# Performance work log

Measured on AMD Instinct MI355X. Metric: run time of the kernel, lower is better.

## Reference

```python
import jax, jax.numpy as jnp
import numpy as np

B, H, S, Dh = 2, 16, 2048, 64


def setup_inputs() -> dict:
    key = jax.random.key(0)
    kq, kk, kv = jax.random.split(key, 3)
    query = jax.random.normal(kq, (B, H, S, Dh), dtype=jnp.float32)
    k = jax.random.normal(kk, (B, H, S, Dh), dtype=jnp.float32)
    value = jax.random.normal(kv, (B, H, S, Dh), dtype=jnp.float32)
    mask = jnp.zeros((1, 1, S, S), dtype=jnp.float32)
    return {"query": query, "key": k, "value": value, "mask": mask}


def reference(query, key, value, mask):
    # scores: [B,H,S,S]
    dk = jnp.asarray(key.shape[-1], dtype=query.dtype)
    logits = jnp.einsum("bhqd,bhkd->bhqk", query, key) / jnp.sqrt(dk)
    logits = logits + mask * (-1e9)
    attention_weights = jax.nn.softmax(logits, axis=-1)
    output = jnp.einsum("bhqk,bhkd->bhqd", attention_weights, value)
    return (output, attention_weights)
```

## Files before the change

kernel.cpp:

```cpp
#include <hip/hip_runtime.h>
#include <hip/hip_bf16.h>
#include <stdint.h>

typedef __bf16 bf16;
typedef __attribute__((ext_vector_type(8))) __bf16 bf16x8;
typedef __attribute__((ext_vector_type(4))) float f32x4;

constexpr int S   = 2048;
constexpr int DH  = 64;
constexpr int BQ  = 16;
constexpr int NW  = 4;
constexpr int KPW = S / NW;
constexpr int NC  = KPW / 32;


__global__ __launch_bounds__(256)
void attn_fused(const float* __restrict__ Q, const float* __restrict__ K,
                const float* __restrict__ V, const float* __restrict__ Msk,
                float* __restrict__ Out, float* __restrict__ W)
{
    __shared__ float rs[NW][BQ];
    __shared__ float inv[BQ];
    __shared__ float opart[NW][BQ][DH];

    const int tid  = threadIdx.x;
    const int lane = tid & 63;
    const int wave = tid >> 6;
    const int c    = lane & 15;
    const int g    = lane >> 4;

    const int swz = (blockIdx.x & 7) * 512 + (blockIdx.x >> 3);
    const int bh = swz >> 7;
    const int q0 = (swz & 127) * BQ;

    const float* Qb = Q + (size_t)bh * S * DH;
    const float* Kb = K + (size_t)bh * S * DH;
    const float* Vb = V + (size_t)bh * S * DH;

    bf16x8 qlo, qhi;
    {
        const float* qr = Qb + (size_t)(q0 + c) * DH + g * 8;
        f32x4 a0 = *(const f32x4*)(qr);
        f32x4 a1 = *(const f32x4*)(qr + 4);
        f32x4 b0 = *(const f32x4*)(qr + 32);
        f32x4 b1 = *(const f32x4*)(qr + 36);
        #pragma unroll
        for (int j = 0; j < 4; ++j) {
            qlo[j]     = (bf16)a0[j];  qlo[j + 4] = (bf16)a1[j];
            qhi[j]     = (bf16)b0[j];  qhi[j + 4] = (bf16)b1[j];
        }
    }

    const int kbase = wave * KPW;
    const int cperm = 8 * (c >> 2) + (c & 3);
    const float* mrow = Msk + (size_t)(q0 + c) * S;

    bf16x8 pa[NC];
    float s = 0.f;
    #pragma unroll
    for (int kc = 0; kc < NC; ++kc) {
        const int k0 = kbase + kc * 32;
        const float* kr0 = Kb + (size_t)(k0 + cperm) * DH + g * 8;
        const float* kr1 = kr0 + (size_t)4 * DH;
        f32x4 a0 = *(const f32x4*)(kr0);
        f32x4 a1 = *(const f32x4*)(kr0 + 4);
        f32x4 b0 = *(const f32x4*)(kr0 + 32);
        f32x4 b1 = *(const f32x4*)(kr0 + 36);
        f32x4 a2 = *(const f32x4*)(kr1);
        f32x4 a3 = *(const f32x4*)(kr1 + 4);
        f32x4 b2 = *(const f32x4*)(kr1 + 32);
        f32x4 b3 = *(const f32x4*)(kr1 + 36);
        f32x4 m0 = *(const f32x4*)(mrow + k0 + 8 * g);
        f32x4 m1 = *(const f32x4*)(mrow + k0 + 8 * g + 4);

        bf16x8 kl0, kh0, kl1, kh1;
        #pragma unroll
        for (int j = 0; j < 4; ++j) {
            kl0[j] = (bf16)a0[j];  kl0[j + 4] = (bf16)a1[j];
            kh0[j] = (bf16)b0[j];  kh0[j + 4] = (bf16)b1[j];
            kl1[j] = (bf16)a2[j];  kl1[j + 4] = (bf16)a3[j];
            kh1[j] = (bf16)b2[j];  kh1[j + 4] = (bf16)b3[j];
        }
        f32x4 acc0 = {0.f, 0.f, 0.f, 0.f};
        f32x4 acc1 = {0.f, 0.f, 0.f, 0.f};
        acc0 = __builtin_amdgcn_mfma_f32_16x16x32_bf16(kl0, qlo, acc0, 0, 0, 0);
        acc0 = __builtin_amdgcn_mfma_f32_16x16x32_bf16(kh0, qhi, acc0, 0, 0, 0);
        acc1 = __builtin_amdgcn_mfma_f32_16x16x32_bf16(kl1, qlo, acc1, 0, 0, 0);
        acc1 = __builtin_amdgcn_mfma_f32_16x16x32_bf16(kh1, qhi, acc1, 0, 0, 0);

        #pragma unroll
        for (int r = 0; r < 4; ++r) {
            const float p0 = __expf(acc0[r] * 0.125f + m0[r] * (-1e9f));
            const float p1 = __expf(acc1[r] * 0.125f + m1[r] * (-1e9f));
            s += p0 + p1;
            pa[kc][r]     = (bf16)p0;
            pa[kc][r + 4] = (bf16)p1;
        }
    }

    s += __shfl_xor(s, 16);
    s += __shfl_xor(s, 32);
    if (lane < 16) rs[wave][lane] = s;
    __syncthreads();
    if (tid < BQ) {
        float t = 0.f;
        #pragma unroll
        for (int w = 0; w < NW; ++w) t += rs[w][tid];
        inv[tid] = 1.f / t;
    }
    __syncthreads();
    const float myinv = inv[c];

    f32x4 oacc[4] = {{0,0,0,0},{0,0,0,0},{0,0,0,0},{0,0,0,0}};
    float* Wrow = W + (size_t)bh * S * S + (size_t)(q0 + c) * S;

    #pragma unroll
    for (int kc = 0; kc < NC; ++kc) {
        const int k0 = kbase + kc * 32;

        const float* vp = Vb + (size_t)(k0 + 8 * g) * DH + c;
        float vv[4][8];
        #pragma unroll
        for (int j = 0; j < 8; ++j) {
            #pragma unroll
            for (int dt = 0; dt < 4; ++dt)
                vv[dt][j] = vp[j * DH + dt * 16];
        }

        f32x4 w0, w1;
        #pragma unroll
        for (int r = 0; r < 4; ++r) {
            w0[r] = (float)pa[kc][r]     * myinv;
            w1[r] = (float)pa[kc][r + 4] * myinv;
        }
        *(f32x4*)(Wrow + k0 + 8 * g)     = w0;
        *(f32x4*)(Wrow + k0 + 8 * g + 4) = w1;

        #pragma unroll
        for (int dt = 0; dt < 4; ++dt) {
            bf16x8 vb;
            #pragma unroll
            for (int j = 0; j < 8; ++j) vb[j] = (bf16)vv[dt][j];
            oacc[dt] = __builtin_amdgcn_mfma_f32_16x16x32_bf16(pa[kc], vb, oacc[dt], 0, 0, 0);
        }
    }

    #pragma unroll
    for (int dt = 0; dt < 4; ++dt)
        #pragma unroll
        for (int r = 0; r < 4; ++r)
            opart[wave][4 * g + r][16 * dt + c] = oacc[dt][r];
    __syncthreads();

    {
        const int q = tid >> 4;
        const int d = (tid & 15) * 4;
        f32x4 o = {0.f, 0.f, 0.f, 0.f};
        #pragma unroll
        for (int w = 0; w < NW; ++w) o += *(const f32x4*)&opart[w][q][d];
        const float is = inv[q];
        o.x *= is; o.y *= is; o.z *= is; o.w *= is;
        float* Ob = Out + ((size_t)bh * S + q0 + q) * DH + d;
        *(f32x4*)Ob = o;
    }
}

extern "C" void kernel_launch(void* const* d_in, const int* in_sizes, int n_in,
                              void* d_out, int out_size, void* d_ws, size_t ws_size,
                              hipStream_t stream) {
    const float* Q   = (const float*)d_in[0];
    const float* K   = (const float*)d_in[1];
    const float* V   = (const float*)d_in[2];
    const float* Msk = (const float*)d_in[3];

    float* Out = (float*)d_out;
    float* W   = Out + (size_t)2 * 16 * 2048 * 64;

    dim3 grid(32 * (S / BQ));
    dim3 block(256);
    hipLaunchKernelGGL(attn_fused, grid, block, 0, stream, Q, K, V, Msk, Out, W);
}
```

Baseline: 440.2 us.

## Pre-cast Q/K to bf16 and pre-transpose V in workspace before attention

Adds two preprocessing kernels: one converts K and Q to bf16, the other converts V to bf16 and transposes it to [bh][d][s]. The main attention kernel then loads bf16 operands directly with vector loads, including contiguous V^T rows for the PV MFMA. This removes the repeated fp32 loads and conversions of K and V, which every query block performs again, and the strided scalar V gathers. The cost is two extra kernel launches and an extra global round trip through workspace, and the old fp32 path is kept as a fallback when the workspace is too small.

Result: faster. 366.2 us (median of 2 runs) (-16.8%).

```diff
diff --git a/kernel.cpp b/kernel.cpp
--- a/kernel.cpp
+++ b/kernel.cpp
@@ -12,12 +12,199 @@
 constexpr int NW  = 4;
 constexpr int KPW = S / NW;
 constexpr int NC  = KPW / 32;
+constexpr int BH  = 32;
+constexpr size_t ELEMS = (size_t)BH * S * DH;
+constexpr size_t WS_NEED = ELEMS * 2 * 3;
 
 
 __global__ __launch_bounds__(256)
-void attn_fused(const float* __restrict__ Q, const float* __restrict__ K,
-                const float* __restrict__ V, const float* __restrict__ Msk,
-                float* __restrict__ Out, float* __restrict__ W)
+void cast_kq(const float* __restrict__ K, const float* __restrict__ Q,
+             bf16* __restrict__ Kb, bf16* __restrict__ Qb)
+{
+    const size_t t = (size_t)blockIdx.x * 256 + threadIdx.x;
+    {
+        const float* src = K + t * 8;
+        f32x4 a = *(const f32x4*)(src);
+        f32x4 b = *(const f32x4*)(src + 4);
+        bf16x8 o;
+        #pragma unroll
+        for (int j = 0; j < 4; ++j) { o[j] = (bf16)a[j]; o[j + 4] = (bf16)b[j]; }
+        *(bf16x8*)(Kb + t * 8) = o;
+    }
+    {
+        const float* src = Q + t * 8;
+        f32x4 a = *(const f32x4*)(src);
+        f32x4 b = *(const f32x4*)(src + 4);
+        bf16x8 o;
+        #pragma unroll
+        for (int j = 0; j < 4; ++j) { o[j] = (bf16)a[j]; o[j + 4] = (bf16)b[j]; }
+        *(bf16x8*)(Qb + t * 8) = o;
+    }
+}
+
+__global__ __launch_bounds__(256)
+void transpose_v(const float* __restrict__ V, bf16* __restrict__ Vt)
+{
+    __shared__ bf16 t[64][72];
+    const int bh = blockIdx.x >> 5;
+    const int sb = (blockIdx.x & 31) * 64;
+    const int tid = threadIdx.x;
+
+    {
+        const int r  = tid >> 2;
+        const int c0 = (tid & 3) * 16;
+        const float* src = V + ((size_t)bh * S + sb + r) * DH + c0;
+        f32x4 v0 = *(const f32x4*)(src);
+        f32x4 v1 = *(const f32x4*)(src + 4);
+        f32x4 v2 = *(const f32x4*)(src + 8);
+        f32x4 v3 = *(const f32x4*)(src + 12);
+        #pragma unroll
+        for (int j = 0; j < 4; ++j) {
+            t[r][c0 + j]      = (bf16)v0[j];
+            t[r][c0 + 4 + j]  = (bf16)v1[j];
+            t[r][c0 + 8 + j]  = (bf16)v2[j];
+            t[r][c0 + 12 + j] = (bf16)v3[j];
+        }
+    }
+    __syncthreads();
+    {
+        const int d  = tid >> 2;
+        const int s0 = (tid & 3) * 16;
+        bf16x8 o0, o1;
+        #pragma unroll
+        for (int j = 0; j < 8; ++j) { o0[j] = t[s0 + j][d]; o1[j] = t[s0 + 8 + j][d]; }
+        bf16* dst = Vt + ((size_t)bh * DH + d) * S + sb + s0;
+        *(bf16x8*)(dst)     = o0;
+        *(bf16x8*)(dst + 8) = o1;
+    }
+}
+
+__global__ __launch_bounds__(256)
+void attn_fused_b16(const bf16* __restrict__ Qb, const bf16* __restrict__ Kb,
+                    const bf16* __restrict__ Vt, const float* __restrict__ Msk,
+                    float* __restrict__ Out, float* __restrict__ W)
+{
+    __shared__ float rs[NW][BQ];
+    __shared__ float inv[BQ];
+    __shared__ float opart[NW][BQ][DH];
+
+    const int tid  = threadIdx.x;
+    const int lane = tid & 63;
+    const int wave = tid >> 6;
+    const int c    = lane & 15;
+    const int g    = lane >> 4;
+
+    const int swz = (blockIdx.x & 7) * 512 + (blockIdx.x >> 3);
+    const int bh = swz >> 7;
+    const int q0 = (swz & 127) * BQ;
+
+    const bf16* Qbb = Qb + (size_t)bh * S * DH;
+    const bf16* Kbb = Kb + (size_t)bh * S * DH;
+    const bf16* Vtb = Vt + (size_t)bh * DH * S;
+
+    const bf16* qr = Qbb + (size_t)(q0 + c) * DH + g * 8;
+    bf16x8 qlo = *(const bf16x8*)(qr);
+    bf16x8 qhi = *(const bf16x8*)(qr + 32);
+
+    const int kbase = wave * KPW;
+    const int cperm = 8 * (c >> 2) + (c & 3);
+    const float* mrow = Msk + (size_t)(q0 + c) * S;
+
+    bf16x8 pa[NC];
+    float s = 0.f;
+    #pragma unroll
+    for (int kc = 0; kc < NC; ++kc) {
+        const int k0 = kbase + kc * 32;
+        const bf16* kr = Kbb + (size_t)(k0 + cperm) * DH + g * 8;
+        bf16x8 kl0 = *(const bf16x8*)(kr);
+        bf16x8 kh0 = *(const bf16x8*)(kr + 32);
+        bf16x8 kl1 = *(const bf16x8*)(kr + 4 * DH);
+        bf16x8 kh1 = *(const bf16x8*)(kr + 4 * DH + 32);
+        f32x4 m0 = *(const f32x4*)(mrow + k0 + 8 * g);
+        f32x4 m1 = *(const f32x4*)(mrow + k0 + 8 * g + 4);
+
+        f32x4 acc0 = {0.f, 0.f, 0.f, 0.f};
+        f32x4 acc1 = {0.f, 0.f, 0.f, 0.f};
+        acc0 = __builtin_amdgcn_mfma_f32_16x16x32_bf16(kl0, qlo, acc0, 0, 0, 0);
+        acc0 = __builtin_amdgcn_mfma_f32_16x16x32_bf16(kh0, qhi, acc0, 0, 0, 0);
+        acc1 = __builtin_amdgcn_mfma_f32_16x16x32_bf16(kl1, qlo, acc1, 0, 0, 0);
+        acc1 = __builtin_amdgcn_mfma_f32_16x16x32_bf16(kh1, qhi, acc1, 0, 0, 0);
+
+        #pragma unroll
+        for (int r = 0; r < 4; ++r) {
+            const float p0 = __expf(acc0[r] * 0.125f + m0[r] * (-1e9f));
+            const float p1 = __expf(acc1[r] * 0.125f + m1[r] * (-1e9f));
+            s += p0 + p1;
+            pa[kc][r]     = (bf16)p0;
+            pa[kc][r + 4] = (bf16)p1;
+        }
+    }
+
+    s += __shfl_xor(s, 16);
+    s += __shfl_xor(s, 32);
+    if (lane < 16) rs[wave][lane] = s;
+    __syncthreads();
+    if (tid < BQ) {
+        float t = 0.f;
+        #pragma unroll
+        for (int w = 0; w < NW; ++w) t += rs[w][tid];
+        inv[tid] = 1.f / t;
+    }
+    __syncthreads();
+    const float myinv = inv[c];
+
+    f32x4 oacc[4] = {{0,0,0,0},{0,0,0,0},{0,0,0,0},{0,0,0,0}};
+    float* Wrow = W + (size_t)bh * S * S + (size_t)(q0 + c) * S;
+
+    #pragma unroll
+    for (int kc = 0; kc < NC; ++kc) {
+        const int k0 = kbase + kc * 32;
+
+        const bf16* vp = Vtb + (size_t)c * S + k0 + 8 * g;
+        bf16x8 vb0 = *(const bf16x8*)(vp);
+        bf16x8 vb1 = *(const bf16x8*)(vp + (size_t)16 * S);
+        bf16x8 vb2 = *(const bf16x8*)(vp + (size_t)32 * S);
+        bf16x8 vb3 = *(const bf16x8*)(vp + (size_t)48 * S);
+
+        f32x4 w0, w1;
+        #pragma unroll
+        for (int r = 0; r < 4; ++r) {
+            w0[r] = (float)pa[kc][r]     * myinv;
+            w1[r] = (float)pa[kc][r + 4] * myinv;
+        }
+        *(f32x4*)(Wrow + k0 + 8 * g)     = w0;
+        *(f32x4*)(Wrow + k0 + 8 * g + 4) = w1;
+
+        oacc[0] = __builtin_amdgcn_mfma_f32_16x16x32_bf16(pa[kc], vb0, oacc[0], 0, 0, 0);
+        oacc[1] = __builtin_amdgcn_mfma_f32_16x16x32_bf16(pa[kc], vb1, oacc[1], 0, 0, 0);
+        oacc[2] = __builtin_amdgcn_mfma_f32_16x16x32_bf16(pa[kc], vb2, oacc[2], 0, 0, 0);
+        oacc[3] = __builtin_amdgcn_mfma_f32_16x16x32_bf16(pa[kc], vb3, oacc[3], 0, 0, 0);
+    }
+
+    #pragma unroll
+    for (int dt = 0; dt < 4; ++dt)
+        #pragma unroll
+        for (int r = 0; r < 4; ++r)
+            opart[wave][4 * g + r][16 * dt + c] = oacc[dt][r];
+    __syncthreads();
+
+    {
+        const int q = tid >> 4;
+        const int d = (tid & 15) * 4;
+        f32x4 o = {0.f, 0.f, 0.f, 0.f};
+        #pragma unroll
+        for (int w = 0; w < NW; ++w) o += *(const f32x4*)&opart[w][q][d];
+        const float is = inv[q];
+        o.x *= is; o.y *= is; o.z *= is; o.w *= is;
+        float* Ob = Out + ((size_t)bh * S + q0 + q) * DH + d;
+        *(f32x4*)Ob = o;
+    }
+}
+
+__global__ __launch_bounds__(256)
+void attn_fused_f32(const float* __restrict__ Q, const float* __restrict__ K,
+                    const float* __restrict__ V, const float* __restrict__ Msk,
+                    float* __restrict__ Out, float* __restrict__ W)
 {
     __shared__ float rs[NW][BQ];
     __shared__ float inv[BQ];
@@ -117,7 +304,6 @@
     #pragma unroll
     for (int kc = 0; kc < NC; ++kc) {
         const int k0 = kbase + kc * 32;
-
         const float* vp = Vb + (size_t)(k0 + 8 * g) * DH + c;
         float vv[4][8];
         #pragma unroll
@@ -126,7 +312,6 @@
             for (int dt = 0; dt < 4; ++dt)
                 vv[dt][j] = vp[j * DH + dt * 16];
         }
-
         f32x4 w0, w1;
         #pragma unroll
         for (int r = 0; r < 4; ++r) {
@@ -176,7 +361,18 @@
     float* Out = (float*)d_out;
     float* W   = Out + (size_t)2 * 16 * 2048 * 64;
 
-    dim3 grid(32 * (S / BQ));
-    dim3 block(256);
-    hipLaunchKernelGGL(attn_fused, grid, block, 0, stream, Q, K, V, Msk, Out, W);
-}
+    if (ws_size >= WS_NEED) {
+        bf16* Kb = (bf16*)d_ws;
+        bf16* Vt = Kb + ELEMS;
+        bf16* Qb = Vt + ELEMS;
+        hipLaunchKernelGGL(cast_kq, dim3(ELEMS / 8 / 256), dim3(256), 0, stream,
+                           K, Q, Kb, Qb);
+        hipLaunchKernelGGL(transpose_v, dim3(BH * (S / 64)), dim3(256), 0, stream,
+                           V, Vt);
+        hipLaunchKernelGGL(attn_fused_b16, dim3(BH * (S / BQ)), dim3(256), 0, stream,
+                           Qb, Kb, Vt, Msk, Out, W);
+    } else {
+        hipLaunchKernelGGL(attn_fused_f32, dim3(BH * (S / BQ)), dim3(256), 0, stream,
+                           Q, K, V, Msk, Out, W);
+    }
+}
```
